# Performance work log

Hardware: AMD Instinct MI355X
Metric: run time of the kernel (lower is better)

The kernel has to match this reference:

```python
import jax, jax.numpy as jnp
import numpy as np
from functools import partial


def deform_sample(inp, dy, dx):
    """Bilinear sample inp[b,c] at (y+dy[b,c,y,x], x+dx[b,c,y,x]) with zero padding.
    inp, dy, dx: [B, C, H, W] -> [B, C, H, W]. Matches torchvision deform_conv2d
    with 1x1 kernel and offset_groups == C (one offset pair per channel)."""
    B, C, H, W = inp.shape
    ys = jnp.arange(H, dtype=inp.dtype)[None, None, :, None] + dy  # [B,C,H,W]
    xs = jnp.arange(W, dtype=inp.dtype)[None, None, None, :] + dx
    y0f = jnp.floor(ys)
    x0f = jnp.floor(xs)
    wy = ys - y0f
    wx = xs - x0f
    y0 = y0f.astype(jnp.int32)
    x0 = x0f.astype(jnp.int32)
    flat = inp.reshape(B, C, H * W)

    def gather(yi, xi):
        valid = (yi >= 0) & (yi < H) & (xi >= 0) & (xi < W)
        idx = jnp.clip(yi, 0, H - 1) * W + jnp.clip(xi, 0, W - 1)
        v = jnp.take_along_axis(flat, idx.reshape(B, C, H * W), axis=2).reshape(B, C, H, W)
        return jnp.where(valid, v, jnp.zeros((), inp.dtype))

    return ((1 - wy) * (1 - wx) * gather(y0, x0)
            + (1 - wy) * wx * gather(y0, x0 + 1)
            + wy * (1 - wx) * gather(y0 + 1, x0)
            + wy * wx * gather(y0 + 1, x0 + 1))


def atm_layer(x, offset, w_weight, w_bias, h_weight, h_bias, local_weight, local_bias,
              fc1_w, fc1_b, fc2_w, fc2_b, proj_w, proj_b):
    B, H, W, C = x.shape
    x_nchw = jnp.transpose(x, (0, 3, 1, 2))  # [B,C,H,W]
    zeros = jnp.zeros_like(x_nchw)

    # ATM along w: offset[:, :C] is x-offset (offset_t[:,1::2]), y-offset 0
    sw = deform_sample(x_nchw, zeros, offset[:, :C])
    w = jnp.einsum('bchw,oc->bhwo', sw, w_weight) + w_bias  # [B,H,W,C]

    # ATM along h: offset[:, C:] is y-offset (offset_t[:,0::2]), x-offset 0
    sh = deform_sample(x_nchw, offset[:, C:], zeros)
    h = jnp.einsum('bchw,oc->bhwo', sh, h_weight) + h_bias

    # depthwise 5x5 conv, padding 2
    c = jax.lax.conv_general_dilated(
        x_nchw, local_weight, window_strides=(1, 1), padding=((2, 2), (2, 2)),
        feature_group_count=C, dimension_numbers=('NCHW', 'OIHW', 'NCHW'))
    c = jnp.transpose(c, (0, 2, 3, 1)) + local_bias  # [B,H,W,C]

    # gating MLP: global average -> fc1 -> GELU -> fc2 -> softmax over 3 branches
    a = (w + h + c).mean(axis=(1, 2))  # [B,C]
    a = jax.nn.gelu(a @ fc1_w.T + fc1_b, approximate=False)
    a = a @ fc2_w.T + fc2_b  # [B,3C]
    a = jnp.transpose(a.reshape(B, C, 3), (2, 0, 1))  # [3,B,C]
    a = jax.nn.softmax(a, axis=0)[:, :, None, None, :]  # [3,B,1,1,C]

    out = w * a[0] + h * a[1] + c * a[2]
    out = out @ proj_w.T + proj_b
    return out


def setup_inputs() -> dict:
    C = 256
    B, H, W = 16, 64, 64
    key = jax.random.key(0)
    ks = jax.random.split(key, 16)
    bnd = 1.0 / np.sqrt(C)
    hid = C // 4
    return {
        'x': jax.random.normal(ks[0], (B, H, W, C), jnp.float32),
        'offset': jax.random.normal(ks[1], (B, 2 * C, H, W), jnp.float32),
        'w_weight': jax.random.uniform(ks[2], (C, C), jnp.float32, -bnd, bnd),
        'w_bias': jax.random.uniform(ks[3], (C,), jnp.float32, -bnd, bnd),
        'h_weight': jax.random.uniform(ks[4], (C, C), jnp.float32, -bnd, bnd),
        'h_bias': jax.random.uniform(ks[5], (C,), jnp.float32, -bnd, bnd),
        'local_weight': jax.random.uniform(ks[6], (C, 1, 5, 5), jnp.float32, -0.2, 0.2),
        'local_bias': jax.random.uniform(ks[7], (C,), jnp.float32, -0.2, 0.2),
        'fc1_w': jax.random.uniform(ks[8], (hid, C), jnp.float32, -bnd, bnd),
        'fc1_b': jax.random.uniform(ks[9], (hid,), jnp.float32, -bnd, bnd),
        'fc2_w': jax.random.uniform(ks[10], (3 * C, hid), jnp.float32, -1.0 / np.sqrt(hid), 1.0 / np.sqrt(hid)),
        'fc2_b': jax.random.uniform(ks[11], (3 * C,), jnp.float32, -1.0 / np.sqrt(hid), 1.0 / np.sqrt(hid)),
        'proj_w': jax.random.uniform(ks[12], (C, C), jnp.float32, -bnd, bnd),
        'proj_b': jax.random.uniform(ks[13], (C,), jnp.float32, -bnd, bnd),
    }


def reference(x, offset, w_weight, w_bias, h_weight, h_bias, local_weight, local_bias,
              fc1_w, fc1_b, fc2_w, fc2_b, proj_w, proj_b):
    return atm_layer(x, offset, w_weight, w_bias, h_weight, h_bias, local_weight,
                     local_bias, fc1_w, fc1_b, fc2_w, fc2_b, proj_w, proj_b)
```

## Files before the change

### kernel.cpp

```cpp
#include <hip/hip_runtime.h>
#include <hip/hip_bf16.h>

typedef _Float16 half4_t __attribute__((ext_vector_type(4)));
typedef _Float16 half8 __attribute__((ext_vector_type(8)));
typedef float f32x4 __attribute__((ext_vector_type(4)));

#define BB 16
#define HH 64
#define WW2 64
#define CC 256

__global__ __launch_bounds__(256) void k_trans(const float* __restrict__ off,
                                               _Float16* __restrict__ offAT,
                                               _Float16* __restrict__ offBT)
{
  __shared__ _Float16 tile[64][65];
  const int blk = blockIdx.x;
  const int st   = blk & 63;
  const int cht  = (blk >> 6) & 3;
  const int half = (blk >> 8) & 1;
  const int b    = blk >> 9;
  const int t = threadIdx.x;

  const int s0 = st * 64;
  const int ch0 = half * 256 + cht * 64;
  const float* src = off + ((size_t)b * 512 + ch0) * 4096 + s0;
  const int sl = t & 63;
  #pragma unroll
  for (int p = 0; p < 16; p++) {
    int chl = (t >> 6) + p * 4;
    tile[chl][sl] = (_Float16)src[(size_t)chl * 4096 + sl];
  }
  __syncthreads();

  _Float16* dst = (half == 0) ? offAT : offBT;
  #pragma unroll
  for (int p = 0; p < 2; p++) {
    int pl = (t >> 3) + p * 32;
    int c8 = (t & 7) * 8;
    half8 hv;
    #pragma unroll
    for (int r = 0; r < 8; r++) hv[r] = tile[c8 + r][pl];
    int s = s0 + pl;
    size_t pix = (half == 0) ? ((size_t)b * 4096 + s)
                             : ((size_t)b * 4096 + (s & 63) * 64 + (s >> 6));
    *(half8*)(dst + pix * 256 + cht * 64 + c8) = hv;
  }
}

__global__ __launch_bounds__(256) void k_rows(
    const float* __restrict__ x, const _Float16* __restrict__ offA,
    _Float16* __restrict__ swb, float* __restrict__ ssw)
{
  __shared__ _Float16 xr[WW2 * CC];

  const int work = (blockIdx.x & 7) * 128 + (blockIdx.x >> 3);
  const int b = work >> 6, y = work & 63;
  const int t = threadIdx.x;
  const int c = t;

  const float* xrow_src = x + (size_t)(b * HH + y) * WW2 * CC;
  #pragma unroll
  for (int p = 0; p < 16; p++) {
    int i = p * 1024 + t * 4;
    float4 v = *(const float4*)(xrow_src + i);
    half4_t h = {(_Float16)v.x, (_Float16)v.y, (_Float16)v.z, (_Float16)v.w};
    *(half4_t*)(xr + i) = h;
  }
  __syncthreads();

  const _Float16* op = offA + ((size_t)b * 4096 + y * 64) * CC + c;
  _Float16* sp = swb + ((size_t)b * 4096 + y * 64) * CC + c;
  float asw = 0.f;

  #pragma unroll 8
  for (int xi = 0; xi < 64; xi++) {
    float dx = (float)op[(size_t)xi * CC];
    float xs = (float)xi + dx;
    float xf = floorf(xs);
    float wx = xs - xf;
    int xq = (int)xf;
    float v0 = (xq >= 0 && xq < WW2) ? (float)xr[xq * CC + c] : 0.f;
    float v1 = (xq + 1 >= 0 && xq + 1 < WW2) ? (float)xr[(xq + 1) * CC + c] : 0.f;
    float swv = (1.f - wx) * v0 + wx * v1;
    sp[(size_t)xi * CC] = (_Float16)swv;
    asw += swv;
  }
  atomicAdd(&ssw[b * CC + c], asw);
}

__global__ __launch_bounds__(256) void k_conv(
    const float* __restrict__ x, const float* __restrict__ lw,
    _Float16* __restrict__ cvb, float* __restrict__ scv)
{
  const int work = (blockIdx.x & 7) * 128 + (blockIdx.x >> 3);
  const int b = work >> 6, y = work & 63;
  const int c = threadIdx.x;

  float wgt[25];
  #pragma unroll
  for (int q = 0; q < 25; q++) wgt[q] = lw[c * 25 + q];

  const float* xb = x + (size_t)b * HH * WW2 * CC + c;
  const float* rp[5];
  bool yv[5];
  #pragma unroll
  for (int ky = 0; ky < 5; ky++) {
    int yy = y + ky - 2;
    yv[ky] = (yy >= 0 && yy < HH);
    rp[ky] = xb + (size_t)(yv[ky] ? yy : 0) * WW2 * CC;
  }

  _Float16* cp = cvb + ((size_t)b * 4096 + y * 64) * CC + c;
  float acc5[5] = {0.f, 0.f, 0.f, 0.f, 0.f};
  float acv = 0.f;

  #pragma unroll 5
  for (int u = 0; u < 70; ++u) {
    acc5[(u + 2) % 5] = 0.f;
    if (u < 64) {
      float c0 = yv[0] ? rp[0][u * CC] : 0.f;
      float c1 = yv[1] ? rp[1][u * CC] : 0.f;
      float c2 = yv[2] ? rp[2][u * CC] : 0.f;
      float c3 = yv[3] ? rp[3][u * CC] : 0.f;
      float c4 = yv[4] ? rp[4][u * CC] : 0.f;
      #pragma unroll
      for (int kx = 0; kx < 5; kx++) {
        acc5[(u + 7 - kx) % 5] += wgt[0 + kx] * c0 + wgt[5 + kx] * c1 +
                                  wgt[10 + kx] * c2 + wgt[15 + kx] * c3 +
                                  wgt[20 + kx] * c4;
      }
    }
    int xi = u - 2;
    if (xi >= 0 && xi < 64) {
      float cv = acc5[(u + 3) % 5];
      cp[(size_t)xi * CC] = (_Float16)cv;
      acv += cv;
    }
  }
  atomicAdd(&scv[b * CC + c], acv);
}

__global__ __launch_bounds__(256) void k_col(
    const float* __restrict__ x, const _Float16* __restrict__ offBT,
    _Float16* __restrict__ shb, float* __restrict__ ssh)
{
  __shared__ _Float16 xc[HH * CC];
  const int work = (blockIdx.x & 7) * 128 + (blockIdx.x >> 3);
  const int b = work >> 6, xi = work & 63;
  const int t = threadIdx.x;
  const int c = t;

  #pragma unroll
  for (int p = 0; p < 16; p++) {
    int yy = p * 4 + (t >> 6);
    int c4 = (t & 63) * 4;
    float4 v = *(const float4*)(x + ((size_t)(b * HH + yy) * WW2 + xi) * CC + c4);
    half4_t h = {(_Float16)v.x, (_Float16)v.y, (_Float16)v.z, (_Float16)v.w};
    *(half4_t*)(xc + yy * CC + c4) = h;
  }
  __syncthreads();

  const _Float16* obt = offBT + ((size_t)(b * WW2 + xi) * HH) * CC + c;
  _Float16* hp = shb + ((size_t)(b * HH) * WW2 + xi) * CC + c;
  float ash = 0.f;
  #pragma unroll 8
  for (int yy = 0; yy < 64; yy++) {
    float dy = (float)obt[(size_t)yy * CC];
    float ys = (float)yy + dy;
    float yf = floorf(ys);
    float wy = ys - yf;
    int yq = (int)yf;
    float u0 = (yq >= 0 && yq < HH) ? (float)xc[yq * CC + c] : 0.f;
    float u1 = (yq + 1 >= 0 && yq + 1 < HH) ? (float)xc[(yq + 1) * CC + c] : 0.f;
    float shv = (1.f - wy) * u0 + wy * u1;
    hp[(size_t)yy * WW2 * CC] = (_Float16)shv;
    ash += shv;
  }
  atomicAdd(&ssh[b * CC + c], ash);
}

__global__ __launch_bounds__(256) void k_gate(
    const float* __restrict__ ssw, const float* __restrict__ ssh, const float* __restrict__ scv,
    const float* __restrict__ Ww, const float* __restrict__ bw,
    const float* __restrict__ Wh, const float* __restrict__ bh,
    const float* __restrict__ blc,
    const float* __restrict__ fc1w, const float* __restrict__ fc1b,
    const float* __restrict__ fc2w, const float* __restrict__ fc2b,
    float* __restrict__ gate)
{
  __shared__ float sswl[CC], sshl[CC], avgl[CC], tl[64];
  const int b = blockIdx.x, tid = threadIdx.x;
  sswl[tid] = ssw[b * CC + tid];
  sshl[tid] = ssh[b * CC + tid];
  __syncthreads();

  float acc = scv[b * CC + tid];
  for (int c = 0; c < CC; c++)
    acc += sswl[c] * Ww[tid * CC + c] + sshl[c] * Wh[tid * CC + c];
  avgl[tid] = acc * (1.f / (HH * WW2)) + bw[tid] + bh[tid] + blc[tid];
  __syncthreads();

  if (tid < 64) {
    float a = fc1b[tid];
    for (int o = 0; o < CC; o++) a += avgl[o] * fc1w[tid * CC + o];
    tl[tid] = 0.5f * a * (1.f + erff(a * 0.70710678118654752f));
  }
  __syncthreads();

  float g[3];
  #pragma unroll
  for (int j = 0; j < 3; j++) {
    float a = fc2b[tid * 3 + j];
    for (int k = 0; k < 64; k++) a += tl[k] * fc2w[(tid * 3 + j) * 64 + k];
    g[j] = a;
  }
  float m = fmaxf(g[0], fmaxf(g[1], g[2]));
  float e0 = expf(g[0] - m), e1 = expf(g[1] - m), e2 = expf(g[2] - m);
  float inv = 1.f / (e0 + e1 + e2);
  gate[(0 * BB + b) * CC + tid] = e0 * inv;
  gate[(1 * BB + b) * CC + tid] = e1 * inv;
  gate[(2 * BB + b) * CC + tid] = e2 * inv;
}

__global__ __launch_bounds__(256) void k_prep(
    const float* __restrict__ gate,
    const float* __restrict__ Ww, const float* __restrict__ Wh,
    const float* __restrict__ bw, const float* __restrict__ bh,
    const float* __restrict__ blc,
    _Float16* __restrict__ Bp, float* __restrict__ bcomb)
{
  const int id = blockIdx.x;
  const int b = id >> 8, n = id & 255;
  const int k = threadIdx.x;
  float a0 = gate[(0 * BB + b) * CC + n];
  float a1 = gate[(1 * BB + b) * CC + n];
  float a2 = gate[(2 * BB + b) * CC + n];
  size_t base = (size_t)id * 512;
  Bp[base + k]       = (_Float16)(a0 * Ww[n * CC + k]);
  Bp[base + 256 + k] = (_Float16)(a1 * Wh[n * CC + k]);
  if (k == 0) bcomb[id] = a0 * bw[n] + a1 * bh[n] + a2 * blc[n];
}

__global__ __launch_bounds__(256) void k_cvt(const float* __restrict__ pw,
                                             _Float16* __restrict__ pf)
{
  int i = blockIdx.x * 256 + threadIdx.x;
  pf[i] = (_Float16)pw[i];
}

#define APAD 264
#define CPAD 260
__global__ __launch_bounds__(256) void k_fused(
    const _Float16* __restrict__ swb, const _Float16* __restrict__ shb,
    const _Float16* __restrict__ Bp, const float* __restrict__ bcomb,
    const float* __restrict__ a2g, const _Float16* __restrict__ cvb,
    const _Float16* __restrict__ pf, const float* __restrict__ pb,
    float* __restrict__ out)
{
  __shared__ _Float16 smem[2 * 64 * APAD];

  const int work = (blockIdx.x & 7) * 128 + (blockIdx.x >> 3);
  const int r0 = work * 64;
  const int b = work >> 6;
  const int tid = threadIdx.x;
  const int wid = tid >> 6, l = tid & 63;
  const int n0 = wid * 64;
  const int lr = l & 15;
  const int kg = (l >> 4) * 8;
  const int jr = (l >> 4) * 4;

  {
    const _Float16* gsw = swb + (size_t)r0 * CC;
    const _Float16* gsh = shb + (size_t)r0 * CC;
    #pragma unroll
    for (int p = 0; p < 8; p++) {
      int i = p * 2048 + tid * 8;
      int row = i >> 8, colp = i & 255;
      half8 v0 = *(const half8*)(gsw + i);
      half8 v1 = *(const half8*)(gsh + i);
      *(half8*)(smem + row * APAD + colp) = v0;
      *(half8*)(smem + 64 * APAD + row * APAD + colp) = v1;
    }
  }
  __syncthreads();

  const _Float16* bp = Bp + ((size_t)b * CC + n0 + lr) * 512 + kg;

  f32x4 acc[4][4];
  #pragma unroll
  for (int mi = 0; mi < 4; mi++)
    #pragma unroll
    for (int ni = 0; ni < 4; ni++) acc[mi][ni] = (f32x4){0.f, 0.f, 0.f, 0.f};

  #pragma unroll
  for (int ks = 0; ks < 16; ks++) {
    const _Float16* abase = (ks < 8) ? smem : (smem + 64 * APAD);
    const int acol = kg + (ks & 7) * 32;
    half8 a[4], bbv[4];
    #pragma unroll
    for (int mi = 0; mi < 4; mi++)
      a[mi] = *(const half8*)(abase + (mi * 16 + lr) * APAD + acol);
    #pragma unroll
    for (int ni = 0; ni < 4; ni++)
      bbv[ni] = *(const half8*)(bp + (size_t)ni * 16 * 512 + ks * 32);
    #pragma unroll
    for (int mi = 0; mi < 4; mi++)
      #pragma unroll
      for (int ni = 0; ni < 4; ni++)
        acc[mi][ni] = __builtin_amdgcn_mfma_f32_16x16x32_f16(a[mi], bbv[ni], acc[mi][ni], 0, 0, 0);
  }

  __syncthreads();

  _Float16* comb = smem;
  #pragma unroll
  for (int ni = 0; ni < 4; ni++) {
    int col = n0 + ni * 16 + lr;
    float bc = bcomb[b * CC + col];
    float a2 = a2g[b * CC + col];
    #pragma unroll
    for (int mi = 0; mi < 4; mi++) {
      #pragma unroll
      for (int j = 0; j < 4; j++) {
        int r = mi * 16 + jr + j;
        size_t idx = (size_t)(r0 + r) * CC + col;
        float v = acc[mi][ni][j] + bc + a2 * (float)cvb[idx];
        comb[r * CPAD + col] = (_Float16)v;
      }
    }
  }
  __syncthreads();

  const _Float16* bp2 = pf + (size_t)(n0 + lr) * CC + kg;

  f32x4 acc2[4][4];
  #pragma unroll
  for (int mi = 0; mi < 4; mi++)
    #pragma unroll
    for (int ni = 0; ni < 4; ni++) acc2[mi][ni] = (f32x4){0.f, 0.f, 0.f, 0.f};

  #pragma unroll
  for (int ks = 0; ks < 8; ks++) {
    half8 a[4], bbv[4];
    #pragma unroll
    for (int mi = 0; mi < 4; mi++) {
      const _Float16* s = comb + (mi * 16 + lr) * CPAD + kg + ks * 32;
      half4_t lo = *(const half4_t*)(s);
      half4_t hi = *(const half4_t*)(s + 4);
      a[mi][0] = lo[0]; a[mi][1] = lo[1]; a[mi][2] = lo[2]; a[mi][3] = lo[3];
      a[mi][4] = hi[0]; a[mi][5] = hi[1]; a[mi][6] = hi[2]; a[mi][7] = hi[3];
    }
    #pragma unroll
    for (int ni = 0; ni < 4; ni++)
      bbv[ni] = *(const half8*)(bp2 + (size_t)ni * 16 * CC + ks * 32);
    #pragma unroll
    for (int mi = 0; mi < 4; mi++)
      #pragma unroll
      for (int ni = 0; ni < 4; ni++)
        acc2[mi][ni] = __builtin_amdgcn_mfma_f32_16x16x32_f16(a[mi], bbv[ni], acc2[mi][ni], 0, 0, 0);
  }

  #pragma unroll
  for (int ni = 0; ni < 4; ni++) {
    int col = n0 + ni * 16 + lr;
    float bias = pb[col];
    #pragma unroll
    for (int mi = 0; mi < 4; mi++) {
      #pragma unroll
      for (int j = 0; j < 4; j++) {
        size_t idx = (size_t)(r0 + mi * 16 + jr + j) * CC + col;
        out[idx] = acc2[mi][ni][j] + bias;
      }
    }
  }
}

extern "C" void kernel_launch(void* const* d_in, const int* in_sizes, int n_in,
                              void* d_out, int out_size, void* d_ws, size_t ws_size,
                              hipStream_t stream)
{
  const float* x    = (const float*)d_in[0];
  const float* off  = (const float*)d_in[1];
  const float* Ww   = (const float*)d_in[2];
  const float* bw   = (const float*)d_in[3];
  const float* Wh   = (const float*)d_in[4];
  const float* bh   = (const float*)d_in[5];
  const float* lw   = (const float*)d_in[6];
  const float* blc  = (const float*)d_in[7];
  const float* fc1w = (const float*)d_in[8];
  const float* fc1b = (const float*)d_in[9];
  const float* fc2w = (const float*)d_in[10];
  const float* fc2b = (const float*)d_in[11];
  const float* pw   = (const float*)d_in[12];
  const float* pb   = (const float*)d_in[13];
  float* out = (float*)d_out;

  char* ws = (char*)d_ws;
  _Float16* shb   = (_Float16*)(ws + 0);
  _Float16* offAT = (_Float16*)(ws + 33554432);
  _Float16* cvb   = (_Float16*)(ws + 33554432);
  _Float16* offBT = (_Float16*)(ws + 67108864);
  _Float16* swb   = (_Float16*)(ws + 67108864);
  _Float16* Bp    = (_Float16*)(ws + 100663296);
  _Float16* pf    = (_Float16*)(ws + 104857600);
  float* sums     = (float*)(ws + 104988672);
  float* gate     = (float*)(ws + 105037824);
  float* bcomb    = (float*)(ws + 105086976);
  float* ssw = sums, *ssh = sums + 4096, *scv = sums + 8192;

  hipMemsetAsync(sums, 0, 3 * 4096 * sizeof(float), stream);
  k_trans<<<8192, 256, 0, stream>>>(off, offAT, offBT);
  k_col<<<BB * WW2, 256, 0, stream>>>(x, offBT, shb, ssh);
  k_rows<<<BB * HH, 256, 0, stream>>>(x, offAT, swb, ssw);
  k_conv<<<BB * HH, 256, 0, stream>>>(x, lw, cvb, scv);
  k_gate<<<BB, 256, 0, stream>>>(ssw, ssh, scv, Ww, bw, Wh, bh, blc,
                                 fc1w, fc1b, fc2w, fc2b, gate);
  k_prep<<<BB * CC, 256, 0, stream>>>(gate, Ww, Wh, bw, bh, blc, Bp, bcomb);
  k_cvt<<<CC, 256, 0, stream>>>(pw, pf);
  k_fused<<<1024, 256, 0, stream>>>(swb, shb, Bp, bcomb, gate + 2 * BB * CC,
                                    cvb, pf, pb, out);
}
```

Baseline: 293.8 us.

## Fold projection weights into per-batch gated matrices and run single K=768 GEMM

Precomputes per-batch combined matrices proj_w·diag(gate)·W for the w and h branches in a new small MFMA kernel, plus a folded output bias. The main kernel then becomes one GEMM over the concatenated sw/sh/conv inputs, dropping the intermediate combine-and-reproject stage and its shared-memory round trip. The three A tiles are streamed through a single shared buffer with register prefetch. Scratch buffers are placed in the output tensor before it is overwritten. The risk is extra fp16 rounding from scaling the weights before conversion.

Measured after the change: 285.2 us. 2.9% less time.

```diff
diff --git a/kernel.cpp b/kernel.cpp
--- a/kernel.cpp
+++ b/kernel.cpp
@@ -45,6 +45,34 @@
     size_t pix = (half == 0) ? ((size_t)b * 4096 + s)
                              : ((size_t)b * 4096 + (s & 63) * 64 + (s >> 6));
     *(half8*)(dst + pix * 256 + cht * 64 + c8) = hv;
+  }
+}
+
+__global__ __launch_bounds__(256) void k_matsT(
+    const float* __restrict__ Ww, const float* __restrict__ Wh,
+    _Float16* __restrict__ WwT, _Float16* __restrict__ WhT)
+{
+  __shared__ _Float16 tile[64][65];
+  const int blk = blockIdx.x;
+  const int nt = blk & 3, kt = (blk >> 2) & 3, mat = blk >> 4;
+  const float* src = mat ? Wh : Ww;
+  _Float16* dst = mat ? WhT : WwT;
+  const int n0 = nt * 64, k0 = kt * 64;
+  const int t = threadIdx.x, sl = t & 63;
+  #pragma unroll
+  for (int p = 0; p < 16; p++) {
+    int chl = (t >> 6) + p * 4;
+    tile[chl][sl] = (_Float16)src[(size_t)(n0 + chl) * 256 + k0 + sl];
+  }
+  __syncthreads();
+  #pragma unroll
+  for (int p = 0; p < 2; p++) {
+    int pl = (t >> 3) + p * 32;
+    int c8 = (t & 7) * 8;
+    half8 hv;
+    #pragma unroll
+    for (int r = 0; r < 8; r++) hv[r] = tile[c8 + r][pl];
+    *(half8*)(dst + (size_t)(k0 + pl) * 256 + n0 + c8) = hv;
   }
 }
 
@@ -187,7 +215,7 @@
     const float* __restrict__ blc,
     const float* __restrict__ fc1w, const float* __restrict__ fc1b,
     const float* __restrict__ fc2w, const float* __restrict__ fc2b,
-    float* __restrict__ gate)
+    _Float16* __restrict__ gh, float* __restrict__ bcomb)
 {
   __shared__ float sswl[CC], sshl[CC], avgl[CC], tl[64];
   const int b = blockIdx.x, tid = threadIdx.x;
@@ -218,28 +246,11 @@
   float m = fmaxf(g[0], fmaxf(g[1], g[2]));
   float e0 = expf(g[0] - m), e1 = expf(g[1] - m), e2 = expf(g[2] - m);
   float inv = 1.f / (e0 + e1 + e2);
-  gate[(0 * BB + b) * CC + tid] = e0 * inv;
-  gate[(1 * BB + b) * CC + tid] = e1 * inv;
-  gate[(2 * BB + b) * CC + tid] = e2 * inv;
-}
-
-__global__ __launch_bounds__(256) void k_prep(
-    const float* __restrict__ gate,
-    const float* __restrict__ Ww, const float* __restrict__ Wh,
-    const float* __restrict__ bw, const float* __restrict__ bh,
-    const float* __restrict__ blc,
-    _Float16* __restrict__ Bp, float* __restrict__ bcomb)
-{
-  const int id = blockIdx.x;
-  const int b = id >> 8, n = id & 255;
-  const int k = threadIdx.x;
-  float a0 = gate[(0 * BB + b) * CC + n];
-  float a1 = gate[(1 * BB + b) * CC + n];
-  float a2 = gate[(2 * BB + b) * CC + n];
-  size_t base = (size_t)id * 512;
-  Bp[base + k]       = (_Float16)(a0 * Ww[n * CC + k]);
-  Bp[base + 256 + k] = (_Float16)(a1 * Wh[n * CC + k]);
-  if (k == 0) bcomb[id] = a0 * bw[n] + a1 * bh[n] + a2 * blc[n];
+  float a0 = e0 * inv, a1 = e1 * inv, a2 = e2 * inv;
+  gh[(0 * BB + b) * CC + tid] = (_Float16)a0;
+  gh[(1 * BB + b) * CC + tid] = (_Float16)a1;
+  gh[(2 * BB + b) * CC + tid] = (_Float16)a2;
+  bcomb[b * CC + tid] = a0 * bw[tid] + a1 * bh[tid] + a2 * blc[tid];
 }
 
 __global__ __launch_bounds__(256) void k_cvt(const float* __restrict__ pw,
@@ -249,16 +260,88 @@
   pf[i] = (_Float16)pw[i];
 }
 
+__global__ __launch_bounds__(256) void k_mats(
+    const _Float16* __restrict__ pf, const _Float16* __restrict__ gh,
+    const _Float16* __restrict__ WwT, const _Float16* __restrict__ WhT,
+    const float* __restrict__ bcomb, const float* __restrict__ pb,
+    _Float16* __restrict__ Bcat, float* __restrict__ bias_out)
+{
+  const int blk = (blockIdx.x & 7) * 16 + (blockIdx.x >> 3);
+  const int ob = blk & 3;
+  const int br = (blk >> 2) & 1;
+  const int b  = blk >> 3;
+  const int o0 = ob * 64;
+  const int tid = threadIdx.x;
+  const int wid = tid >> 6, l = tid & 63;
+  const int n0 = wid * 64;
+  const int lr = l & 15;
+  const int kg = (l >> 4) * 8;
+  const int jr = (l >> 4) * 4;
+
+  const _Float16* WT  = br ? WhT : WwT;
+  const _Float16* ghb = gh + (size_t)(br * BB + b) * CC;
+
+  f32x4 acc[4][4];
+  #pragma unroll
+  for (int mi = 0; mi < 4; mi++)
+    #pragma unroll
+    for (int ni = 0; ni < 4; ni++) acc[mi][ni] = (f32x4){0.f, 0.f, 0.f, 0.f};
+
+  #pragma unroll
+  for (int ks = 0; ks < 8; ks++) {
+    half8 gv = *(const half8*)(ghb + kg + ks * 32);
+    half8 a[4], bbv[4];
+    #pragma unroll
+    for (int mi = 0; mi < 4; mi++)
+      a[mi] = *(const half8*)(pf + (size_t)(o0 + mi * 16 + lr) * CC + kg + ks * 32) * gv;
+    #pragma unroll
+    for (int ni = 0; ni < 4; ni++)
+      bbv[ni] = *(const half8*)(WT + (size_t)(n0 + ni * 16 + lr) * CC + kg + ks * 32);
+    #pragma unroll
+    for (int mi = 0; mi < 4; mi++)
+      #pragma unroll
+      for (int ni = 0; ni < 4; ni++)
+        acc[mi][ni] = __builtin_amdgcn_mfma_f32_16x16x32_f16(a[mi], bbv[ni], acc[mi][ni], 0, 0, 0);
+  }
+
+  #pragma unroll
+  for (int ni = 0; ni < 4; ni++) {
+    int kcol = n0 + ni * 16 + lr;
+    #pragma unroll
+    for (int mi = 0; mi < 4; mi++) {
+      #pragma unroll
+      for (int j = 0; j < 4; j++) {
+        int o = o0 + mi * 16 + jr + j;
+        Bcat[((size_t)b * CC + o) * 512 + br * 256 + kcol] = (_Float16)acc[mi][ni][j];
+      }
+    }
+  }
+
+  if (br == 0) {
+    int o_l = tid >> 2, part = tid & 3;
+    const _Float16* pr = pf + (size_t)(o0 + o_l) * CC + part * 64;
+    const float* bc = bcomb + b * CC + part * 64;
+    float s = 0.f;
+    #pragma unroll
+    for (int i = 0; i < 8; i++) {
+      half8 h = *(const half8*)(pr + i * 8);
+      #pragma unroll
+      for (int r = 0; r < 8; r++) s += (float)h[r] * bc[i * 8 + r];
+    }
+    s += __shfl_xor(s, 1);
+    s += __shfl_xor(s, 2);
+    if (part == 0) bias_out[b * CC + o0 + o_l] = s + pb[o0 + o_l];
+  }
+}
+
 #define APAD 264
-#define CPAD 260
-__global__ __launch_bounds__(256) void k_fused(
+__global__ __launch_bounds__(256) void k_gemm(
     const _Float16* __restrict__ swb, const _Float16* __restrict__ shb,
-    const _Float16* __restrict__ Bp, const float* __restrict__ bcomb,
-    const float* __restrict__ a2g, const _Float16* __restrict__ cvb,
-    const _Float16* __restrict__ pf, const float* __restrict__ pb,
-    float* __restrict__ out)
-{
-  __shared__ _Float16 smem[2 * 64 * APAD];
+    const _Float16* __restrict__ cvb, const _Float16* __restrict__ Bcat,
+    const _Float16* __restrict__ pf, const _Float16* __restrict__ a2h,
+    const float* __restrict__ bias_out, float* __restrict__ out)
+{
+  __shared__ _Float16 smem[64 * APAD];
 
   const int work = (blockIdx.x & 7) * 128 + (blockIdx.x >> 3);
   const int r0 = work * 64;
@@ -270,107 +353,108 @@
   const int kg = (l >> 4) * 8;
   const int jr = (l >> 4) * 4;
 
+  const _Float16* bq = Bcat + ((size_t)b * CC + n0 + lr) * 512 + kg;
+
+  f32x4 acc[4][4];
+  #pragma unroll
+  for (int mi = 0; mi < 4; mi++)
+    #pragma unroll
+    for (int ni = 0; ni < 4; ni++) acc[mi][ni] = (f32x4){0.f, 0.f, 0.f, 0.f};
+
+  half8 st[8];
   {
-    const _Float16* gsw = swb + (size_t)r0 * CC;
-    const _Float16* gsh = shb + (size_t)r0 * CC;
+    const _Float16* g = swb + (size_t)r0 * CC;
+    #pragma unroll
+    for (int p = 0; p < 8; p++) st[p] = *(const half8*)(g + p * 2048 + tid * 8);
     #pragma unroll
     for (int p = 0; p < 8; p++) {
       int i = p * 2048 + tid * 8;
-      int row = i >> 8, colp = i & 255;
-      half8 v0 = *(const half8*)(gsw + i);
-      half8 v1 = *(const half8*)(gsh + i);
-      *(half8*)(smem + row * APAD + colp) = v0;
-      *(half8*)(smem + 64 * APAD + row * APAD + colp) = v1;
+      *(half8*)(smem + (i >> 8) * APAD + (i & 255)) = st[p];
     }
   }
   __syncthreads();
-
-  const _Float16* bp = Bp + ((size_t)b * CC + n0 + lr) * 512 + kg;
-
-  f32x4 acc[4][4];
-  #pragma unroll
-  for (int mi = 0; mi < 4; mi++)
-    #pragma unroll
-    for (int ni = 0; ni < 4; ni++) acc[mi][ni] = (f32x4){0.f, 0.f, 0.f, 0.f};
-
-  #pragma unroll
-  for (int ks = 0; ks < 16; ks++) {
-    const _Float16* abase = (ks < 8) ? smem : (smem + 64 * APAD);
-    const int acol = kg + (ks & 7) * 32;
+  {
+    const _Float16* g = shb + (size_t)r0 * CC;
+    #pragma unroll
+    for (int p = 0; p < 8; p++) st[p] = *(const half8*)(g + p * 2048 + tid * 8);
+  }
+  #pragma unroll
+  for (int ks = 0; ks < 8; ks++) {
     half8 a[4], bbv[4];
     #pragma unroll
     for (int mi = 0; mi < 4; mi++)
-      a[mi] = *(const half8*)(abase + (mi * 16 + lr) * APAD + acol);
+      a[mi] = *(const half8*)(smem + (mi * 16 + lr) * APAD + kg + ks * 32);
     #pragma unroll
     for (int ni = 0; ni < 4; ni++)
-      bbv[ni] = *(const half8*)(bp + (size_t)ni * 16 * 512 + ks * 32);
+      bbv[ni] = *(const half8*)(bq + (size_t)ni * 16 * 512 + ks * 32);
     #pragma unroll
     for (int mi = 0; mi < 4; mi++)
       #pragma unroll
       for (int ni = 0; ni < 4; ni++)
         acc[mi][ni] = __builtin_amdgcn_mfma_f32_16x16x32_f16(a[mi], bbv[ni], acc[mi][ni], 0, 0, 0);
   }
-
-  __syncthreads();
-
-  _Float16* comb = smem;
+  __syncthreads();
+  #pragma unroll
+  for (int p = 0; p < 8; p++) {
+    int i = p * 2048 + tid * 8;
+    *(half8*)(smem + (i >> 8) * APAD + (i & 255)) = st[p];
+  }
+  __syncthreads();
+  {
+    const _Float16* g = cvb + (size_t)r0 * CC;
+    #pragma unroll
+    for (int p = 0; p < 8; p++) st[p] = *(const half8*)(g + p * 2048 + tid * 8);
+  }
+  #pragma unroll
+  for (int ks = 0; ks < 8; ks++) {
+    half8 a[4], bbv[4];
+    #pragma unroll
+    for (int mi = 0; mi < 4; mi++)
+      a[mi] = *(const half8*)(smem + (mi * 16 + lr) * APAD + kg + ks * 32);
+    #pragma unroll
+    for (int ni = 0; ni < 4; ni++)
+      bbv[ni] = *(const half8*)(bq + (size_t)ni * 16 * 512 + 256 + ks * 32);
+    #pragma unroll
+    for (int mi = 0; mi < 4; mi++)
+      #pragma unroll
+      for (int ni = 0; ni < 4; ni++)
+        acc[mi][ni] = __builtin_amdgcn_mfma_f32_16x16x32_f16(a[mi], bbv[ni], acc[mi][ni], 0, 0, 0);
+  }
+  __syncthreads();
+  #pragma unroll
+  for (int p = 0; p < 8; p++) {
+    int i = p * 2048 + tid * 8;
+    *(half8*)(smem + (i >> 8) * APAD + (i & 255)) = st[p];
+  }
+  __syncthreads();
+  const _Float16* a2b = a2h + (size_t)b * CC;
+  #pragma unroll
+  for (int ks = 0; ks < 8; ks++) {
+    half8 a2v = *(const half8*)(a2b + kg + ks * 32);
+    half8 a[4], bbv[4];
+    #pragma unroll
+    for (int mi = 0; mi < 4; mi++)
+      a[mi] = *(const half8*)(smem + (mi * 16 + lr) * APAD + kg + ks * 32);
+    #pragma unroll
+    for (int ni = 0; ni < 4; ni++)
+      bbv[ni] = *(const half8*)(pf + (size_t)(n0 + ni * 16 + lr) * CC + kg + ks * 32) * a2v;
+    #pragma unroll
+    for (int mi = 0; mi < 4; mi++)
+      #pragma unroll
+      for (int ni = 0; ni < 4; ni++)
+        acc[mi][ni] = __builtin_amdgcn_mfma_f32_16x16x32_f16(a[mi], bbv[ni], acc[mi][ni], 0, 0, 0);
+  }
+
   #pragma unroll
   for (int ni = 0; ni < 4; ni++) {
     int col = n0 + ni * 16 + lr;
-    float bc = bcomb[b * CC + col];
-    float a2 = a2g[b * CC + col];
-    #pragma unroll
-    for (int mi = 0; mi < 4; mi++) {
-      #pragma unroll
-      for (int j = 0; j < 4; j++) {
-        int r = mi * 16 + jr + j;
-        size_t idx = (size_t)(r0 + r) * CC + col;
-        float v = acc[mi][ni][j] + bc + a2 * (float)cvb[idx];
-        comb[r * CPAD + col] = (_Float16)v;
-      }
-    }
-  }
-  __syncthreads();
-
-  const _Float16* bp2 = pf + (size_t)(n0 + lr) * CC + kg;
-
-  f32x4 acc2[4][4];
-  #pragma unroll
-  for (int mi = 0; mi < 4; mi++)
-    #pragma unroll
-    for (int ni = 0; ni < 4; ni++) acc2[mi][ni] = (f32x4){0.f, 0.f, 0.f, 0.f};
-
-  #pragma unroll
-  for (int ks = 0; ks < 8; ks++) {
-    half8 a[4], bbv[4];
-    #pragma unroll
-    for (int mi = 0; mi < 4; mi++) {
-      const _Float16* s = comb + (mi * 16 + lr) * CPAD + kg + ks * 32;
-      half4_t lo = *(const half4_t*)(s);
-      half4_t hi = *(const half4_t*)(s + 4);
-      a[mi][0] = lo[0]; a[mi][1] = lo[1]; a[mi][2] = lo[2]; a[mi][3] = lo[3];
-      a[mi][4] = hi[0]; a[mi][5] = hi[1]; a[mi][6] = hi[2]; a[mi][7] = hi[3];
-    }
-    #pragma unroll
-    for (int ni = 0; ni < 4; ni++)
-      bbv[ni] = *(const half8*)(bp2 + (size_t)ni * 16 * CC + ks * 32);
-    #pragma unroll
-    for (int mi = 0; mi < 4; mi++)
-      #pragma unroll
-      for (int ni = 0; ni < 4; ni++)
-        acc2[mi][ni] = __builtin_amdgcn_mfma_f32_16x16x32_f16(a[mi], bbv[ni], acc2[mi][ni], 0, 0, 0);
-  }
-
-  #pragma unroll
-  for (int ni = 0; ni < 4; ni++) {
-    int col = n0 + ni * 16 + lr;
-    float bias = pb[col];
+    float bo = bias_out[b * CC + col];
     #pragma unroll
     for (int mi = 0; mi < 4; mi++) {
       #pragma unroll
       for (int j = 0; j < 4; j++) {
         size_t idx = (size_t)(r0 + mi * 16 + jr + j) * CC + col;
-        out[idx] = acc2[mi][ni][j] + bias;
+        out[idx] = acc[mi][ni][j] + bo;
       }
     }
   }
@@ -402,22 +486,26 @@
   _Float16* cvb   = (_Float16*)(ws + 33554432);
   _Float16* offBT = (_Float16*)(ws + 67108864);
   _Float16* swb   = (_Float16*)(ws + 67108864);
-  _Float16* Bp    = (_Float16*)(ws + 100663296);
+  _Float16* Bcat  = (_Float16*)(ws + 100663296);
   _Float16* pf    = (_Float16*)(ws + 104857600);
-  float* sums     = (float*)(ws + 104988672);
-  float* gate     = (float*)(ws + 105037824);
-  float* bcomb    = (float*)(ws + 105086976);
+  _Float16* gh    = (_Float16*)(ws + 104988672);
+  float* bcomb    = (float*)(ws + 105013248);
+  float* bias_out = (float*)(ws + 105029632);
+  _Float16* WwT = (_Float16*)((char*)d_out + 0);
+  _Float16* WhT = (_Float16*)((char*)d_out + 131072);
+  float* sums   = (float*)((char*)d_out + 262144);
   float* ssw = sums, *ssh = sums + 4096, *scv = sums + 8192;
 
   hipMemsetAsync(sums, 0, 3 * 4096 * sizeof(float), stream);
+  k_matsT<<<32, 256, 0, stream>>>(Ww, Wh, WwT, WhT);
   k_trans<<<8192, 256, 0, stream>>>(off, offAT, offBT);
   k_col<<<BB * WW2, 256, 0, stream>>>(x, offBT, shb, ssh);
   k_rows<<<BB * HH, 256, 0, stream>>>(x, offAT, swb, ssw);
   k_conv<<<BB * HH, 256, 0, stream>>>(x, lw, cvb, scv);
   k_gate<<<BB, 256, 0, stream>>>(ssw, ssh, scv, Ww, bw, Wh, bh, blc,
-                                 fc1w, fc1b, fc2w, fc2b, gate);
-  k_prep<<<BB * CC, 256, 0, stream>>>(gate, Ww, Wh, bw, bh, blc, Bp, bcomb);
+                                 fc1w, fc1b, fc2w, fc2b, gh, bcomb);
   k_cvt<<<CC, 256, 0, stream>>>(pw, pf);
-  k_fused<<<1024, 256, 0, stream>>>(swb, shb, Bp, bcomb, gate + 2 * BB * CC,
-                                    cvb, pf, pb, out);
-}
+  k_mats<<<128, 256, 0, stream>>>(pf, gh, WwT, WhT, bcomb, pb, Bcat, bias_out);
+  k_gemm<<<1024, 256, 0, stream>>>(swb, shb, cvb, Bcat, pf, gh + 2 * BB * CC,
+                                   bias_out, out);
+}
```
